# Performance work log

Hardware: AMD Instinct MI355X
Metric: run time of the kernel (lower is better)

## Reference

```python
import jax, jax.numpy as jnp
import numpy as np


def setup_inputs() -> dict:
    key = jax.random.key(0)
    kz, kh, k0 = jax.random.split(key, 3)
    B, C, D, H, W = 2, 96, 32, 32, 32
    z = jax.random.uniform(kz, (B, C, D, H, W), dtype=jnp.float32)  # gate in [0,1]
    h_tilde = jax.random.normal(kh, (B, C, D, H, W), dtype=jnp.float32)  # candidate state
    h0 = jax.random.uniform(k0, (1,), dtype=jnp.float32)  # scalar initial state
    return {"z": z, "h_tilde": h_tilde, "h0": h0}


def reference(z, h_tilde, h0):
    """GruDirection3d with d1=d2=d3=1 (forward_3, no flips).

    The three wavefront slice-updates in the torch code jointly implement
        out[d, y, x] = z[d, y, x] * h_tilde[d, y, x]
                       + (1 - z[d, y, x]) * out[d-1, y-1, x-1]
    with out == h0 whenever any index goes below 0 (the padded border).
    We realize it as t_num = min(D, H, W) full-volume shifted updates: after
    iteration k, all voxels with min(d, y, x) <= k-1 hold their final value,
    so after t_num iterations the result matches the torch wavefront DP exactly.
    """
    B, C, D, H, W = z.shape
    t_num = min(D, H, W)  # static shapes -> python int, jit-safe
    # padded state: index 0 along each spatial axis is the h0 border (never written)
    h_pad = jnp.full((B, C, D + 1, H + 1, W + 1), h0[0], dtype=z.dtype)

    one = jnp.asarray(1, dtype=z.dtype)

    def step(h_pad, _):
        prev = h_pad[:, :, :-1, :-1, :-1]  # out[d-1, y-1, x-1] (with border = h0)
        new = z * h_tilde + (one - z) * prev
        return h_pad.at[:, :, 1:, 1:, 1:].set(new), None

    h_pad, _ = jax.lax.scan(step, h_pad, None, length=t_num)
    return h_pad[:, :, 1:, 1:, 1:]
```

## Files before the change

kernel.cpp:

```cpp
#include <hip/hip_runtime.h>


#define PLANE 1024
#define DD 32

__global__ __launch_bounds__(1024) void gru3d_preload(
    const float* __restrict__ z,
    const float* __restrict__ ht,
    const float* __restrict__ h0p,
    float* __restrict__ out)
{
    __shared__ float buf[2][PLANE];

    const int bc  = blockIdx.x;
    const int tid = threadIdx.x;
    const int y   = tid >> 5;
    const int x   = tid & 31;

    const float* zb = z   + (size_t)bc * (DD * PLANE);
    const float* tb = ht  + (size_t)bc * (DD * PLANE);
    float*       ob = out + (size_t)bc * (DD * PLANE);

    const float h0 = h0p[0];

    float zr[DD], tr[DD];
    #pragma unroll
    for (int d = 0; d < DD; ++d) {
        zr[d] = zb[d * PLANE + tid];
        tr[d] = tb[d * PLANE + tid];
    }

    const bool interior = (y > 0) & (x > 0);

    float h = zr[0] * (tr[0] - h0) + h0;
    ob[tid] = h;
    buf[0][tid] = h;
    __syncthreads();

    #pragma unroll
    for (int d = 1; d < DD; ++d) {
        const float pv = interior ? buf[(d - 1) & 1][tid - 33] : h0;
        const float hn = zr[d] * (tr[d] - pv) + pv;
        ob[d * PLANE + tid] = hn;
        buf[d & 1][tid] = hn;
        __syncthreads();
    }
}

extern "C" void kernel_launch(void* const* d_in, const int* in_sizes, int n_in,
                              void* d_out, int out_size, void* d_ws, size_t ws_size,
                              hipStream_t stream) {
    const float* z  = (const float*)d_in[0];
    const float* ht = (const float*)d_in[1];
    const float* h0 = (const float*)d_in[2];
    float* out      = (float*)d_out;

    const int BC = 2 * 96;
    gru3d_preload<<<dim3(BC), dim3(1024), 0, stream>>>(z, ht, h0, out);
}
```

Measured before the change: 95.03 us.

## Walk diagonal lines per thread to remove shared memory and barriers

Each thread now follows one diagonal line (d, a+d, b+d mod 32) through the volume, so the recurrence is carried in a register and needs neither shared memory nor per-plane __syncthreads. Blocks shrink to 256 threads with 4x as many blocks, and loads are software-prefetched 8 planes ahead in a rolling register buffer instead of preloading all 32 planes. Wrapping the coordinates modulo 32 keeps accesses coalesced and resets to h0 at the border; the cost is a border check on every step.

```diff
diff --git a/kernel.cpp b/kernel.cpp
--- a/kernel.cpp
+++ b/kernel.cpp
@@ -1,49 +1,56 @@
 #include <hip/hip_runtime.h>
 
 
-#define PLANE 1024
 #define DD 32
+#define PF 8
 
-__global__ __launch_bounds__(1024) void gru3d_preload(
+__global__ __launch_bounds__(256) void gru3d_helix(
     const float* __restrict__ z,
     const float* __restrict__ ht,
     const float* __restrict__ h0p,
     float* __restrict__ out)
 {
-    __shared__ float buf[2][PLANE];
-
-    const int bc  = blockIdx.x;
-    const int tid = threadIdx.x;
-    const int y   = tid >> 5;
-    const int x   = tid & 31;
-
-    const float* zb = z   + (size_t)bc * (DD * PLANE);
-    const float* tb = ht  + (size_t)bc * (DD * PLANE);
-    float*       ob = out + (size_t)bc * (DD * PLANE);
+    const int blk  = blockIdx.x;
+    const int slab = blk >> 2;
+    const int agrp = blk & 3;
+    const int tid  = threadIdx.x;
+    const int a    = (agrp << 3) + (tid >> 5);
+    const int b    = tid & 31;
 
     const float h0 = h0p[0];
 
-    float zr[DD], tr[DD];
+    const size_t base = (size_t)slab * (DD * 1024);
+    const float* __restrict__ zb = z   + base;
+    const float* __restrict__ tb = ht  + base;
+    float*       __restrict__ ob = out + base;
+
+    auto off = [&](int d) -> int {
+        return (d << 10) | (((a + d) & 31) << 5) | ((b + d) & 31);
+    };
+
+    float zr[PF], tr[PF];
+    #pragma unroll
+    for (int p = 0; p < PF; ++p) {
+        zr[p] = zb[off(p)];
+        tr[p] = tb[off(p)];
+    }
+
+    float h = h0;
+
     #pragma unroll
     for (int d = 0; d < DD; ++d) {
-        zr[d] = zb[d * PLANE + tid];
-        tr[d] = tb[d * PLANE + tid];
-    }
+        const int s = d & (PF - 1);
 
-    const bool interior = (y > 0) & (x > 0);
+        const bool border = (((a + d) & 31) == 0) | (((b + d) & 31) == 0);
+        const float pred  = border ? h0 : h;
 
-    float h = zr[0] * (tr[0] - h0) + h0;
-    ob[tid] = h;
-    buf[0][tid] = h;
-    __syncthreads();
+        h = zr[s] * (tr[s] - pred) + pred;
+        ob[off(d)] = h;
 
-    #pragma unroll
-    for (int d = 1; d < DD; ++d) {
-        const float pv = interior ? buf[(d - 1) & 1][tid - 33] : h0;
-        const float hn = zr[d] * (tr[d] - pv) + pv;
-        ob[d * PLANE + tid] = hn;
-        buf[d & 1][tid] = hn;
-        __syncthreads();
+        if (d + PF < DD) {
+            zr[s] = zb[off(d + PF)];
+            tr[s] = tb[off(d + PF)];
+        }
     }
 }
 
@@ -56,5 +63,5 @@
     float* out      = (float*)d_out;
 
     const int BC = 2 * 96;
-    gru3d_preload<<<dim3(BC), dim3(1024), 0, stream>>>(z, ht, h0, out);
+    gru3d_helix<<<dim3(BC * 4), dim3(256), 0, stream>>>(z, ht, h0, out);
 }
```

Measured after the change: 92.59 us. -2.6%, faster.
